# Kernel optimization log

Measured on AMD Instinct MI355X. Metric: run time of the kernel, lower is better.

The kernel has to match this reference:

```python
import jax, jax.numpy as jnp
import numpy as np

K = 4          # conv kernel size
DIL = 3        # conv dilation
EPS = 1e-5     # rms eps inside gate kernel
NORM_EPS = 1e-5  # RMSNorm eps for value rms


def setup_inputs() -> dict:
    key = jax.random.key(0)
    ks = jax.random.split(key, 10)
    B, T, G, C, E = 2, 4096, 4, 1024, 1024
    return {
        "embeddings": jax.random.normal(ks[0], (B, T, E), jnp.float32),
        "hidden_states": jax.random.normal(ks[1], (B, T, G, C), jnp.float32),
        "key_w": jax.random.normal(ks[2], (G * C, E), jnp.float32) * 0.02,
        "key_b": jax.random.normal(ks[3], (G * C,), jnp.float32) * 0.02,
        "value_w": jax.random.normal(ks[4], (C, E), jnp.float32) * 0.02,
        "value_b": jax.random.normal(ks[5], (C,), jnp.float32) * 0.02,
        "w_key_norm": jax.random.uniform(ks[6], (G, C), jnp.float32, 0.5, 1.5),
        "w_query_norm": jax.random.uniform(ks[7], (G, C), jnp.float32, 0.5, 1.5),
        "w_norm": jax.random.uniform(ks[8], (G, C), jnp.float32, 0.5, 1.5),
        "conv_weight": jax.random.normal(ks[9], (G * C, K), jnp.float32) * 0.1,
    }


def reference(embeddings, hidden_states, key_w, key_b, value_w, value_b,
              w_key_norm, w_query_norm, w_norm, conv_weight):
    B, T, G, C = hidden_states.shape
    # projections
    k_all = (embeddings @ key_w.T + key_b).reshape(B, T, G, C)     # [B,T,G,C]
    q_all = hidden_states                                          # [B,T,G,C]
    vproj = embeddings @ value_w.T + value_b                       # [B,T,C]

    # gate kernel: per (b,t,g) RMS of key/query + weighted dot -> sign-sqrt-sigmoid gate
    rms_k = jnp.sqrt(jnp.mean(k_all * k_all, axis=-1) + EPS)       # [B,T,G]
    rms_q = jnp.sqrt(jnp.mean(q_all * q_all, axis=-1) + EPS)       # [B,T,G]
    dot = jnp.einsum('btgc,gc,btgc,gc->btg', k_all, w_key_norm, q_all, w_query_norm)
    gate_raw = dot / (rms_k * rms_q) / jnp.sqrt(jnp.float32(C))
    gate = jax.nn.sigmoid(jnp.where(gate_raw >= 0, 1.0, -1.0)
                          * jnp.sqrt(jnp.maximum(jnp.abs(gate_raw), 1e-6)))
    value = vproj[:, :, None, :] * gate[..., None]                 # [B,T,G,C]
    rms_v = jnp.sqrt(jnp.mean(value * value, axis=-1) + NORM_EPS)  # [B,T,G]

    # conv+residual kernel: per-group RMS-norm, dilated depthwise causal conv, SiLU, residual
    normed = value * (w_norm[None, None] / rms_v[..., None])       # [B,T,G,C]
    conv_w = conv_weight.reshape(G, C, K)                          # depthwise weights
    pad = (K - 1) * DIL
    xp = jnp.pad(normed, ((0, 0), (pad, 0), (0, 0), (0, 0)))
    # acc[b,t,g,c] = sum_k normed[b, t-(K-1-k)*DIL, g, c] * conv_w[g,c,k]
    acc = xp[:, 0:T] * conv_w[None, None, :, :, 0]
    for k in range(1, K):
        acc = acc + xp[:, k * DIL: k * DIL + T] * conv_w[None, None, :, :, k]
    acc = acc * jax.nn.sigmoid(acc)  # SiLU activation
    return value + acc
```

## Files before the change

kernel.cpp:

```cpp
#include <hip/hip_runtime.h>
#include <hip/hip_bf16.h>
#include <cstdint>
#include <cstddef>

using bf16 = __hip_bfloat16;

typedef __bf16 bf16x8_t __attribute__((ext_vector_type(8)));
typedef float  f32x4_t  __attribute__((ext_vector_type(4)));

static constexpr int Bb = 2;
static constexpr int Tt = 4096;
static constexpr int Gg = 4;
static constexpr int Cc = 1024;
static constexpr int Mm = Bb * Tt;
static constexpr int GC = Gg * Cc;

__device__ __forceinline__ float bfbits2f(unsigned u) {
  union { unsigned i; float f; } c; c.i = u << 16; return c.f;
}
__device__ __forceinline__ ushort f2bfbits(float v) {
  union { __hip_bfloat16 h; ushort u; } c; c.h = __float2bfloat16(v); return c.u;
}

__device__ __forceinline__ void store_val(bf16* p, float v)  { *p = __float2bfloat16(v); }
__device__ __forceinline__ void store_val(float* p, float v) { *p = v; }

__device__ __forceinline__ void gld_lds16(const ushort* g, ushort* l) {
  __builtin_amdgcn_global_load_lds(
      (const __attribute__((address_space(1))) void*)g,
      (__attribute__((address_space(3))) void*)l, 16, 0, 0);
}

__global__ __launch_bounds__(256)
void cvt_bf16(const float* __restrict__ in, ushort* __restrict__ out, int n4)
{
  const int i = blockIdx.x * 256 + threadIdx.x;
  if (i >= n4) return;
  const float4 v = ((const float4*)in)[i];
  ushort4 o;
  o.x = f2bfbits(v.x); o.y = f2bfbits(v.y);
  o.z = f2bfbits(v.z); o.w = f2bfbits(v.w);
  ((ushort4*)out)[i] = o;
}

__global__ __launch_bounds__(256)
void cvt_split(const float* __restrict__ in, ushort* __restrict__ hi,
               ushort* __restrict__ lo, int n4)
{
  const int i = blockIdx.x * 256 + threadIdx.x;
  if (i >= n4) return;
  const float4 v = ((const float4*)in)[i];
  ushort4 h, l;
  h.x = f2bfbits(v.x); l.x = f2bfbits(v.x - bfbits2f(h.x));
  h.y = f2bfbits(v.y); l.y = f2bfbits(v.y - bfbits2f(h.y));
  h.z = f2bfbits(v.z); l.z = f2bfbits(v.z - bfbits2f(h.z));
  h.w = f2bfbits(v.w); l.w = f2bfbits(v.w - bfbits2f(h.w));
  ((ushort4*)hi)[i] = h;
  ((ushort4*)lo)[i] = l;
}

__global__ __launch_bounds__(256, 2)
void gemm_key_fused(const ushort* __restrict__ embH, const ushort* __restrict__ embL,
                    const ushort* __restrict__ kwH,  const ushort* __restrict__ kwL,
                    const float* __restrict__ key_b, const float* __restrict__ hid,
                    const float* __restrict__ wkn,   const float* __restrict__ wqn,
                    float* __restrict__ k2_part, float* __restrict__ dot_part,
                    float* __restrict__ q2_part)
{
  constexpr int K = Cc;
  __shared__ __align__(16) ushort sA[128 * 64];
  __shared__ __align__(16) ushort sB[128 * 64];

  const int tid  = threadIdx.x;
  const int lane = tid & 63;
  const int wave = tid >> 6;
  const int wm   = wave & 1;
  const int wn   = wave >> 1;
  const int row0 = blockIdx.y * 128;
  const int col0 = blockIdx.x * 128;

  const int srow = tid >> 3;
  const int scol = ((tid & 7) ^ (srow & 7)) * 8;
  ushort* aWB = sA + wave * 512;
  ushort* bWB = sB + wave * 512;

  f32x4_t acc[4][4] = {};

  const ushort* Asrc[3] = { embH, embH, embL };
  const ushort* Bsrc[3] = { kwH,  kwL,  kwH  };

  for (int pass = 0; pass < 3; ++pass) {
    const ushort* __restrict__ A  = Asrc[pass];
    const ushort* __restrict__ Bm = Bsrc[pass];
    for (int kt = 0; kt < K; kt += 64) {
#pragma unroll
      for (int p = 0; p < 4; ++p) {
        gld_lds16(A  + (size_t)(row0 + p * 32 + srow) * K + kt + scol,
                  aWB + p * 2048);
        gld_lds16(Bm + (size_t)(col0 + p * 32 + srow) * K + kt + scol,
                  bWB + p * 2048);
      }
      __syncthreads();

#pragma unroll
      for (int ks = 0; ks < 2; ++ks) {
        const int cb  = ks * 4 + (lane >> 4);
        const int ce  = ((cb ^ (lane & 7)) * 8);
        bf16x8_t af[4], bfr[4];
#pragma unroll
        for (int mi = 0; mi < 4; ++mi) {
          const int r = wm * 64 + mi * 16 + (lane & 15);
          af[mi] = *(const bf16x8_t*)(sA + r * 64 + ce);
        }
#pragma unroll
        for (int ni = 0; ni < 4; ++ni) {
          const int r = wn * 64 + ni * 16 + (lane & 15);
          bfr[ni] = *(const bf16x8_t*)(sB + r * 64 + ce);
        }
#pragma unroll
        for (int mi = 0; mi < 4; ++mi)
#pragma unroll
          for (int ni = 0; ni < 4; ++ni)
            acc[mi][ni] = __builtin_amdgcn_mfma_f32_16x16x32_bf16(
                af[mi], bfr[ni], acc[mi][ni], 0, 0, 0);
      }
      __syncthreads();
    }
  }

  const int lrow = lane >> 4;
  const int lcol = lane & 15;
  const int g    = col0 >> 10;

  float s2[4][4] = {};
  float su[4][4] = {};
  float sq[4][4] = {};

#pragma unroll
  for (int ni = 0; ni < 4; ++ni) {
    const int col = col0 + wn * 64 + ni * 16 + lcol;
    const float kb = key_b[col];
    const float ww = wkn[col] * wqn[col];
#pragma unroll
    for (int mi = 0; mi < 4; ++mi) {
      const int rowb = row0 + wm * 64 + mi * 16 + lrow * 4;
#pragma unroll
      for (int r = 0; r < 4; ++r) {
        const float q = hid[(size_t)(rowb + r) * GC + col];
        const float k = acc[mi][ni][r] + kb;
        s2[mi][r] += k * k;
        su[mi][r] += k * ww * q;
        sq[mi][r] += q * q;
      }
    }
  }
#pragma unroll
  for (int off = 1; off < 16; off <<= 1) {
#pragma unroll
    for (int mi = 0; mi < 4; ++mi)
#pragma unroll
      for (int r = 0; r < 4; ++r) {
        s2[mi][r] += __shfl_xor(s2[mi][r], off);
        su[mi][r] += __shfl_xor(su[mi][r], off);
        sq[mi][r] += __shfl_xor(sq[mi][r], off);
      }
  }
  if (lcol == 0) {
#pragma unroll
    for (int mi = 0; mi < 4; ++mi) {
      const int rowb = row0 + wm * 64 + mi * 16 + lrow * 4;
#pragma unroll
      for (int r = 0; r < 4; ++r) {
        atomicAdd(&k2_part[(rowb + r) * Gg + g],  s2[mi][r]);
        atomicAdd(&dot_part[(rowb + r) * Gg + g], su[mi][r]);
        atomicAdd(&q2_part[(rowb + r) * Gg + g],  sq[mi][r]);
      }
    }
  }
}

template <typename OutT>
__global__ __launch_bounds__(256, 2)
void gemm_bt(const ushort* __restrict__ A, const ushort* __restrict__ Bm,
             const float* __restrict__ bias, OutT* __restrict__ C,
             int M, int N, int K)
{
  __shared__ __align__(16) ushort sA[128 * 64];
  __shared__ __align__(16) ushort sB[128 * 64];

  const int tid  = threadIdx.x;
  const int lane = tid & 63;
  const int wave = tid >> 6;
  const int wm   = wave & 1;
  const int wn   = wave >> 1;
  const int row0 = blockIdx.y * 128;
  const int col0 = blockIdx.x * 128;

  const int srow = tid >> 3;
  const int scol = ((tid & 7) ^ (srow & 7)) * 8;
  ushort* aWB = sA + wave * 512;
  ushort* bWB = sB + wave * 512;

  f32x4_t acc[4][4] = {};

  for (int kt = 0; kt < K; kt += 64) {
#pragma unroll
    for (int p = 0; p < 4; ++p) {
      gld_lds16(A  + (size_t)(row0 + p * 32 + srow) * K + kt + scol,
                aWB + p * 2048);
      gld_lds16(Bm + (size_t)(col0 + p * 32 + srow) * K + kt + scol,
                bWB + p * 2048);
    }
    __syncthreads();

#pragma unroll
    for (int ks = 0; ks < 2; ++ks) {
      const int cb = ks * 4 + (lane >> 4);
      const int ce = ((cb ^ (lane & 7)) * 8);
      bf16x8_t af[4], bfr[4];
#pragma unroll
      for (int mi = 0; mi < 4; ++mi) {
        const int r = wm * 64 + mi * 16 + (lane & 15);
        af[mi] = *(const bf16x8_t*)(sA + r * 64 + ce);
      }
#pragma unroll
      for (int ni = 0; ni < 4; ++ni) {
        const int r = wn * 64 + ni * 16 + (lane & 15);
        bfr[ni] = *(const bf16x8_t*)(sB + r * 64 + ce);
      }
#pragma unroll
      for (int mi = 0; mi < 4; ++mi)
#pragma unroll
        for (int ni = 0; ni < 4; ++ni)
          acc[mi][ni] = __builtin_amdgcn_mfma_f32_16x16x32_bf16(
              af[mi], bfr[ni], acc[mi][ni], 0, 0, 0);
    }
    __syncthreads();
  }

  const int lrow = lane >> 4;
  const int lcol = lane & 15;
#pragma unroll
  for (int ni = 0; ni < 4; ++ni) {
    const int col = col0 + wn * 64 + ni * 16 + lcol;
    const float bv = bias[col];
#pragma unroll
    for (int mi = 0; mi < 4; ++mi) {
      const int rowb = row0 + wm * 64 + mi * 16 + lrow * 4;
#pragma unroll
      for (int r = 0; r < 4; ++r)
        store_val(&C[(size_t)(rowb + r) * N + col], acc[mi][ni][r] + bv);
    }
  }
}

__global__ __launch_bounds__(256)
void finalize_kernel(const float* __restrict__ vproj,
                     const float* __restrict__ k2_part,
                     const float* __restrict__ dot_part,
                     const float* __restrict__ q2_part,
                     float* __restrict__ gate_o, float* __restrict__ snorm_o)
{
  const int bt   = blockIdx.x;
  const int tid  = threadIdx.x;
  const int g    = tid >> 6;
  const int lane = tid & 63;

  const float4 v4 = ((const float4*)(vproj + (size_t)bt * Cc))[tid];
  float pv = v4.x * v4.x + v4.y * v4.y + v4.z * v4.z + v4.w * v4.w;
#pragma unroll
  for (int off = 32; off > 0; off >>= 1) pv += __shfl_xor(pv, off);
  __shared__ float wsum[4];
  if (lane == 0) wsum[g] = pv;
  __syncthreads();

  if (lane == 0) {
    const float mv = (wsum[0] + wsum[1] + wsum[2] + wsum[3]) * (1.0f / 1024.0f);
    const float sk = k2_part[bt * Gg + g];
    const float sd = dot_part[bt * Gg + g];
    const float sq = q2_part[bt * Gg + g];
    const float rk = sqrtf(sk * (1.0f / 1024.0f) + 1e-5f);
    const float rq = sqrtf(sq * (1.0f / 1024.0f) + 1e-5f);
    const float graw = sd / (rk * rq) * (1.0f / 32.0f);
    const float sgn = (graw >= 0.f) ? 1.f : -1.f;
    const float gate = 1.f / (1.f + expf(-sgn * sqrtf(fmaxf(fabsf(graw), 1e-6f))));
    const float rv = sqrtf(gate * gate * mv + 1e-5f);
    gate_o[bt * Gg + g]  = gate;
    snorm_o[bt * Gg + g] = gate / rv;
  }
}

static constexpr int CJ  = 128;
static constexpr int NCH = 11;

__global__ __launch_bounds__(256)
void conv_kernel(const float* __restrict__ vproj, const float* __restrict__ gate,
                 const float* __restrict__ snorm, const float* __restrict__ wnm,
                 const float* __restrict__ cw, float* __restrict__ out)
{
  int x = blockIdx.x;
  const int cb = x & 3;  x >>= 2;
  const int p  = x % 3;  x /= 3;
  const int ch = x % NCH; x /= NCH;
  const int g  = x & 3;  x >>= 2;
  const int b  = x;
  const int c  = cb * 256 + threadIdx.x;

  const float wn = wnm[g * Cc + c];
  const float4 w = ((const float4*)cw)[g * Cc + c];

  int t = p + 3 * (ch * CJ);
  if (t >= Tt) return;

  float n1 = 0.f, n2 = 0.f, n3 = 0.f;
#pragma unroll
  for (int h = 3; h >= 1; --h) {
    const int th = t - 3 * h;
    float nv = 0.f;
    if (th >= 0) {
      const int bt = b * Tt + th;
      nv = vproj[(size_t)bt * Cc + c] * snorm[bt * Gg + g] * wn;
    }
    n3 = n2; n2 = n1; n1 = nv;
  }

  for (int j = 0; j < CJ && t < Tt; ++j, t += 3) {
    const int bt = b * Tt + t;
    const float vp  = vproj[(size_t)bt * Cc + c];
    const float gt  = gate[bt * Gg + g];
    const float sn  = snorm[bt * Gg + g];
    const float cur = vp * sn * wn;
    const float a   = w.x * n3 + w.y * n2 + w.z * n1 + w.w * cur;
    const float si  = a / (1.f + __expf(-a));
    out[((size_t)bt * Gg + g) * Cc + c] = vp * gt + si;
    n3 = n2; n2 = n1; n1 = cur;
  }
}

extern "C" void kernel_launch(void* const* d_in, const int* in_sizes, int n_in,
                              void* d_out, int out_size, void* d_ws, size_t ws_size,
                              hipStream_t stream)
{
  const float* emb   = (const float*)d_in[0];
  const float* hid   = (const float*)d_in[1];
  const float* key_w = (const float*)d_in[2];
  const float* key_b = (const float*)d_in[3];
  const float* val_w = (const float*)d_in[4];
  const float* val_b = (const float*)d_in[5];
  const float* wkn   = (const float*)d_in[6];
  const float* wqn   = (const float*)d_in[7];
  const float* wnm   = (const float*)d_in[8];
  const float* cwt   = (const float*)d_in[9];
  float* out = (float*)d_out;

  char* ws = (char*)d_ws;
  ushort* embH  = (ushort*)ws;  ws += (size_t)Mm * Cc * 2;
  ushort* embL  = (ushort*)ws;  ws += (size_t)Mm * Cc * 2;
  ushort* kwH   = (ushort*)ws;  ws += (size_t)GC * Cc * 2;
  ushort* kwL   = (ushort*)ws;  ws += (size_t)GC * Cc * 2;
  ushort* vwB   = (ushort*)ws;  ws += (size_t)Cc * Cc * 2;
  float*  vproj = (float*)ws;   ws += (size_t)Mm * Cc * 4;
  float*  k2p   = (float*)ws;   ws += (size_t)Mm * Gg * 4;
  float*  dotp  = (float*)ws;   ws += (size_t)Mm * Gg * 4;
  float*  q2p   = (float*)ws;   ws += (size_t)Mm * Gg * 4;
  float*  gate  = (float*)ws;   ws += (size_t)Mm * Gg * 4;
  float*  snorm = (float*)ws;

  hipMemsetAsync(k2p, 0, (size_t)3 * Mm * Gg * 4, stream);

  dim3 blk(256);
  cvt_split<<<dim3((Mm * Cc / 4) / 256), blk, 0, stream>>>(emb,   embH, embL, Mm * Cc / 4);
  cvt_split<<<dim3((GC * Cc / 4) / 256), blk, 0, stream>>>(key_w, kwH,  kwL,  GC * Cc / 4);
  cvt_bf16 <<<dim3((Cc * Cc / 4) / 256), blk, 0, stream>>>(val_w, vwB,  Cc * Cc / 4);

  gemm_key_fused<<<dim3(GC / 128, Mm / 128), blk, 0, stream>>>(
      embH, embL, kwH, kwL, key_b, hid, wkn, wqn, k2p, dotp, q2p);

  gemm_bt<float><<<dim3(Cc / 128, Mm / 128), blk, 0, stream>>>(
      embH, vwB, val_b, vproj, Mm, Cc, Cc);

  finalize_kernel<<<dim3(Mm), blk, 0, stream>>>(vproj, k2p, dotp, q2p, gate, snorm);

  const int nblocks = Bb * Gg * NCH * 3 * (Cc / 256);
  conv_kernel<<<dim3(nblocks), blk, 0, stream>>>(vproj, gate, snorm, wnm, cwt, out);
}
```

Baseline: 637.2 us.

## Fuse three split-bf16 GEMM passes into one K loop with hi/lo tiles

The key-projection GEMM used to make three separate passes over K (hi*hi, hi*lo, lo*hi), reloading A and B tiles each pass. It now loads the hi and lo tiles of both operands together per K step and issues all three MFMAs per fragment pair. That cuts global loads from six tile loads to four per K step and removes two thirds of the barriers. In exchange LDS use doubles to 64KB per block and register pressure rises from the extra fragments, which can lower occupancy under launch_bounds(256,2).

```diff
diff --git a/kernel.cpp b/kernel.cpp
--- a/kernel.cpp
+++ b/kernel.cpp
@@ -68,8 +68,10 @@
                     float* __restrict__ q2_part)
 {
   constexpr int K = Cc;
-  __shared__ __align__(16) ushort sA[128 * 64];
-  __shared__ __align__(16) ushort sB[128 * 64];
+  __shared__ __align__(16) ushort sAH[128 * 64];
+  __shared__ __align__(16) ushort sAL[128 * 64];
+  __shared__ __align__(16) ushort sBH[128 * 64];
+  __shared__ __align__(16) ushort sBL[128 * 64];
 
   const int tid  = threadIdx.x;
   const int lane = tid & 63;
@@ -81,51 +83,52 @@
 
   const int srow = tid >> 3;
   const int scol = ((tid & 7) ^ (srow & 7)) * 8;
-  ushort* aWB = sA + wave * 512;
-  ushort* bWB = sB + wave * 512;
+  const int wofs = wave * 512;
 
   f32x4_t acc[4][4] = {};
 
-  const ushort* Asrc[3] = { embH, embH, embL };
-  const ushort* Bsrc[3] = { kwH,  kwL,  kwH  };
-
-  for (int pass = 0; pass < 3; ++pass) {
-    const ushort* __restrict__ A  = Asrc[pass];
-    const ushort* __restrict__ Bm = Bsrc[pass];
-    for (int kt = 0; kt < K; kt += 64) {
-#pragma unroll
-      for (int p = 0; p < 4; ++p) {
-        gld_lds16(A  + (size_t)(row0 + p * 32 + srow) * K + kt + scol,
-                  aWB + p * 2048);
-        gld_lds16(Bm + (size_t)(col0 + p * 32 + srow) * K + kt + scol,
-                  bWB + p * 2048);
-      }
-      __syncthreads();
-
-#pragma unroll
-      for (int ks = 0; ks < 2; ++ks) {
-        const int cb  = ks * 4 + (lane >> 4);
-        const int ce  = ((cb ^ (lane & 7)) * 8);
-        bf16x8_t af[4], bfr[4];
-#pragma unroll
-        for (int mi = 0; mi < 4; ++mi) {
-          const int r = wm * 64 + mi * 16 + (lane & 15);
-          af[mi] = *(const bf16x8_t*)(sA + r * 64 + ce);
+  for (int kt = 0; kt < K; kt += 64) {
+#pragma unroll
+    for (int p = 0; p < 4; ++p) {
+      const size_t aoff = (size_t)(row0 + p * 32 + srow) * K + kt + scol;
+      const size_t boff = (size_t)(col0 + p * 32 + srow) * K + kt + scol;
+      gld_lds16(embH + aoff, sAH + p * 2048 + wofs);
+      gld_lds16(embL + aoff, sAL + p * 2048 + wofs);
+      gld_lds16(kwH  + boff, sBH + p * 2048 + wofs);
+      gld_lds16(kwL  + boff, sBL + p * 2048 + wofs);
+    }
+    __syncthreads();
+
+#pragma unroll
+    for (int ks = 0; ks < 2; ++ks) {
+      const int cb = ks * 4 + (lane >> 4);
+      const int ce = ((cb ^ (lane & 7)) * 8);
+      bf16x8_t afH[4], afL[4], bfH[4], bfL[4];
+#pragma unroll
+      for (int mi = 0; mi < 4; ++mi) {
+        const int r = wm * 64 + mi * 16 + (lane & 15);
+        afH[mi] = *(const bf16x8_t*)(sAH + r * 64 + ce);
+        afL[mi] = *(const bf16x8_t*)(sAL + r * 64 + ce);
+      }
+#pragma unroll
+      for (int ni = 0; ni < 4; ++ni) {
+        const int r = wn * 64 + ni * 16 + (lane & 15);
+        bfH[ni] = *(const bf16x8_t*)(sBH + r * 64 + ce);
+        bfL[ni] = *(const bf16x8_t*)(sBL + r * 64 + ce);
+      }
+#pragma unroll
+      for (int mi = 0; mi < 4; ++mi)
+#pragma unroll
+        for (int ni = 0; ni < 4; ++ni) {
+          acc[mi][ni] = __builtin_amdgcn_mfma_f32_16x16x32_bf16(
+              afH[mi], bfH[ni], acc[mi][ni], 0, 0, 0);
+          acc[mi][ni] = __builtin_amdgcn_mfma_f32_16x16x32_bf16(
+              afH[mi], bfL[ni], acc[mi][ni], 0, 0, 0);
+          acc[mi][ni] = __builtin_amdgcn_mfma_f32_16x16x32_bf16(
+              afL[mi], bfH[ni], acc[mi][ni], 0, 0, 0);
         }
-#pragma unroll
-        for (int ni = 0; ni < 4; ++ni) {
-          const int r = wn * 64 + ni * 16 + (lane & 15);
-          bfr[ni] = *(const bf16x8_t*)(sB + r * 64 + ce);
-        }
-#pragma unroll
-        for (int mi = 0; mi < 4; ++mi)
-#pragma unroll
-          for (int ni = 0; ni < 4; ++ni)
-            acc[mi][ni] = __builtin_amdgcn_mfma_f32_16x16x32_bf16(
-                af[mi], bfr[ni], acc[mi][ni], 0, 0, 0);
-      }
-      __syncthreads();
-    }
+    }
+    __syncthreads();
   }
 
   const int lrow = lane >> 4;
```

After: 600.6 us. 5.7% less time.
